# Performance work log

Hardware: AMD Instinct MI355X
Metric: run time of the kernel (lower is better)

The kernel has to match this reference:

```python
import itertools
import jax, jax.numpy as jnp
import numpy as np


def setup_inputs() -> dict:
    key = jax.random.key(0)
    k1, k2 = jax.random.split(key)
    # vol: [B, D, H, W, C]; flow: [B, D, H, W, 3] (dense displacement field, 'ij' indexing)
    vol = jax.random.normal(k1, (2, 160, 192, 160, 2), dtype=jnp.float32)
    flow = jax.random.normal(k2, (2, 160, 192, 160, 3), dtype=jnp.float32)
    return {"vol": vol, "flow": flow}


def _warp_single(vol, flow):
    """Trilinear warp of one volume. vol: [D,H,W,C], flow: [D,H,W,3]."""
    D, H, W, C = vol.shape
    nb_dims = 3
    # identity grid ('ij' indexing) + displacement -> sample locations
    gd, gh, gw = jnp.meshgrid(jnp.arange(D), jnp.arange(H), jnp.arange(W), indexing="ij")
    mesh = jnp.stack([gd, gh, gw], axis=-1).astype(flow.dtype)  # [D,H,W,3]
    loc = mesh + flow                                            # [D,H,W,3]

    max_loc = jnp.array([D - 1, H - 1, W - 1], dtype=loc.dtype)  # per-dim clamp
    loc0 = jnp.clip(jnp.floor(loc), 0.0, max_loc)                # lower corner (clipped)
    loc1 = jnp.clip(loc0 + 1.0, 0.0, max_loc)                    # upper corner (clipped)

    # linear weights: corner bit 0 -> (loc1 - loc), corner bit 1 -> 1 - (loc1 - loc)
    d1 = loc1 - loc   # weight when picking lower corner
    d0 = 1.0 - d1     # weight when picking upper corner

    i0 = loc0.astype(jnp.int32)  # [D,H,W,3]
    i1 = loc1.astype(jnp.int32)
    strides = (H * W, W, 1)
    vol_flat = vol.reshape(-1, C)  # [D*H*W, C]

    out = jnp.zeros((D, H, W, C), dtype=vol.dtype)
    for corner in itertools.product([0, 1], repeat=nb_dims):
        idx = 0
        wt = 1.0
        for d in range(nb_dims):
            ii = (i1 if corner[d] else i0)[..., d]
            idx = idx + ii * strides[d]
            wt = wt * (d0 if corner[d] else d1)[..., d]
        out = out + wt[..., None] * vol_flat[idx]  # gather [D,H,W,C]
    return out


def reference(vol, flow):
    # batch map over [B, ...] volumes, matching SpatialTransformer.call with a dense flow
    return jax.vmap(_warp_single)(vol, flow)
```

## Files before the change

kernel.cpp:

```cpp
#include <hip/hip_runtime.h>


constexpr int Bb = 2, Dd = 160, Hh = 192, Ww = 160;
constexpr int HW  = Hh * Ww;
constexpr int VOX = Dd * HW;

constexpr int TD = 8,  TH = 16, TW = 16;
constexpr int RD = TD + 8;
constexpr int RH = TH + 8;
constexpr int RW = TW + 8;
constexpr int RWP = 24;
constexpr int QROW = RW / 2;
constexpr int NQ = RD * RH * QROW;
constexpr int ND = Dd / TD, NH = Hh / TH, NW = Ww / TW;
constexpr int NBLK = Bb * ND * NH * NW;
constexpr int BLOCK = 1024;
constexpr size_t LDS_BYTES = (size_t)NQ * 16;

__device__ __forceinline__ void sample_global(const float2* __restrict__ v2,
                                              int d, int h, int w,
                                              float fx, float fy, float fz,
                                              float& oxv, float& oyv)
{
    const float mx = (float)(Dd - 1), my = (float)(Hh - 1), mz = (float)(Ww - 1);
    const float lxf = (float)d + fx;
    const float lyf = (float)h + fy;
    const float lzf = (float)w + fz;

    const float l0x = fminf(fmaxf(floorf(lxf), 0.0f), mx);
    const float l0y = fminf(fmaxf(floorf(lyf), 0.0f), my);
    const float l0z = fminf(fmaxf(floorf(lzf), 0.0f), mz);
    const float l1x = fminf(l0x + 1.0f, mx);
    const float l1y = fminf(l0y + 1.0f, my);
    const float l1z = fminf(l0z + 1.0f, mz);

    const float d1x = l1x - lxf, d0x = 1.0f - d1x;
    const float d1y = l1y - lyf, d0y = 1.0f - d1y;
    const float d1z = l1z - lzf, d0z = 1.0f - d1z;

    const int i0x = (int)l0x, i1x = (int)l1x;
    const int i0y = (int)l0y, i1y = (int)l1y;
    const int i0z = (int)l0z, i1z = (int)l1z;

    const int rx0 = i0x * HW, rx1 = i1x * HW;
    const int ry0 = i0y * Ww, ry1 = i1y * Ww;
    const float2 c000 = v2[rx0 + ry0 + i0z], c001 = v2[rx0 + ry0 + i1z];
    const float2 c010 = v2[rx0 + ry1 + i0z], c011 = v2[rx0 + ry1 + i1z];
    const float2 c100 = v2[rx1 + ry0 + i0z], c101 = v2[rx1 + ry0 + i1z];
    const float2 c110 = v2[rx1 + ry1 + i0z], c111 = v2[rx1 + ry1 + i1z];

    const float w000 = d1x * d1y * d1z, w001 = d1x * d1y * d0z;
    const float w010 = d1x * d0y * d1z, w011 = d1x * d0y * d0z;
    const float w100 = d0x * d1y * d1z, w101 = d0x * d1y * d0z;
    const float w110 = d0x * d0y * d1z, w111 = d0x * d0y * d0z;

    oxv = w000 * c000.x;
    oyv = w000 * c000.y;
    oxv = fmaf(w001, c001.x, oxv);  oyv = fmaf(w001, c001.y, oyv);
    oxv = fmaf(w010, c010.x, oxv);  oyv = fmaf(w010, c010.y, oyv);
    oxv = fmaf(w011, c011.x, oxv);  oyv = fmaf(w011, c011.y, oyv);
    oxv = fmaf(w100, c100.x, oxv);  oyv = fmaf(w100, c100.y, oyv);
    oxv = fmaf(w101, c101.x, oxv);  oyv = fmaf(w101, c101.y, oyv);
    oxv = fmaf(w110, c110.x, oxv);  oyv = fmaf(w110, c110.y, oyv);
    oxv = fmaf(w111, c111.x, oxv);  oyv = fmaf(w111, c111.y, oyv);
}

__global__ __launch_bounds__(BLOCK, 8)
void SpatialTransformer_44418551776013_kernel(const float* __restrict__ vol,
                                              const float* __restrict__ flow,
                                              float* __restrict__ out)
{
    extern __shared__ float2 sv[];
    const int tid = threadIdx.x;

    constexpr int CPX = NBLK / 8;
    int bid = (int)(blockIdx.x % 8) * CPX + (int)(blockIdx.x / 8);

    const int bw = bid % NW;  bid /= NW;
    const int bh = bid % NH;  bid /= NH;
    const int bd = bid % ND;
    const int b  = bid / ND;
    const int d0 = bd * TD, h0 = bh * TH, w0 = bw * TW;

    const int ox = max(0, d0 - 4), oy = max(0, h0 - 4), oz = max(0, w0 - 4);
    const int ex = min(Dd - 1, d0 + TD + 3) - ox + 1;
    const int ey = min(Hh - 1, h0 + TH + 3) - oy + 1;
    const int ez = min(Ww - 1, w0 + TW + 3) - oz + 1;
    const int qz = ez >> 1;

    const int tw2 = tid & 7;
    const int th  = (tid >> 3) & 15;
    const int td  = tid >> 7;
    const int h = h0 + th;
    const int w = w0 + 2 * tw2;
    const int d = d0 + td;
    const int gidx = ((b * Dd + d) * Hh + h) * Ww + w;

    const float4 fA = *reinterpret_cast<const float4*>(flow + (size_t)gidx * 3);
    const float2 fB = *reinterpret_cast<const float2*>(flow + (size_t)gidx * 3 + 4);

    const float2* __restrict__ v2 =
        reinterpret_cast<const float2*>(vol) + (size_t)b * VOX;

    if ((ex == RD) & (ey == RH) & (ez == RW)) {
        #pragma unroll 1
        for (int k = 0; k < 5; ++k) {
            const int i = tid + k * BLOCK;
            if (i < NQ) {
                const int lq = i % QROW;
                const int t  = i / QROW;
                const int ly = t % RH;
                const int lx = t / RH;
                const float2* src =
                    v2 + ((size_t)(ox + lx) * HW + (oy + ly) * Ww + oz + 2 * lq);
                __builtin_amdgcn_global_load_lds(
                    (const __attribute__((address_space(1))) void*)src,
                    (__attribute__((address_space(3))) void*)(sv + (size_t)2 * i),
                    16, 0, 0);
            }
        }
    } else {
        #pragma unroll 1
        for (int k = 0; k < 5; ++k) {
            const int i = tid + k * BLOCK;
            if (i < NQ) {
                int lq = i % QROW;
                const int t  = i / QROW;
                int ly = t % RH;
                int lx = t / RH;
                lx = min(lx, ex - 1);  ly = min(ly, ey - 1);  lq = min(lq, qz - 1);
                const float2* src =
                    v2 + ((size_t)(ox + lx) * HW + (oy + ly) * Ww + oz + 2 * lq);
                __builtin_amdgcn_global_load_lds(
                    (const __attribute__((address_space(1))) void*)src,
                    (__attribute__((address_space(3))) void*)(sv + (size_t)2 * i),
                    16, 0, 0);
            }
        }
    }
    __syncthreads();

    auto sample_lds = [&](int dd, int ww, float fx, float fy, float fz,
                          float& oxv, float& oyv, bool& ok) {
        const float mn3 = fminf(fminf(fx, fy), fz);
        const float mx3 = fmaxf(fmaxf(fx, fy), fz);
        ok = (mn3 >= -4.0f) & (mx3 < 4.0f);

        const float lxf = (float)dd + fx;
        const float lyf = (float)h  + fy;
        const float lzf = (float)ww + fz;

        const int i0x = min(max(__float2int_rd(lxf), 0), Dd - 1);
        const int i0y = min(max(__float2int_rd(lyf), 0), Hh - 1);
        const int i0z = min(max(__float2int_rd(lzf), 0), Ww - 1);
        const int i1x = min(i0x + 1, Dd - 1);
        const int i1y = min(i0y + 1, Hh - 1);
        const int i1z = min(i0z + 1, Ww - 1);

        const float d1x = (float)i1x - lxf, d0x = 1.0f - d1x;
        const float d1y = (float)i1y - lyf, d0y = 1.0f - d1y;
        const float d1z = (float)i1z - lzf, d0z = 1.0f - d1z;

        const int a0x = i0x - ox, a1x = i1x - ox;
        const int a0y = i0y - oy, a1y = i1y - oy;
        const int a0z = i0z - oz, a1z = i1z - oz;

        const int r00 = (a0x * RH + a0y) * RWP;
        const int r01 = (a0x * RH + a1y) * RWP;
        const int r10 = (a1x * RH + a0y) * RWP;
        const int r11 = (a1x * RH + a1y) * RWP;
        const float2 c000 = sv[r00 + a0z], c001 = sv[r00 + a1z];
        const float2 c010 = sv[r01 + a0z], c011 = sv[r01 + a1z];
        const float2 c100 = sv[r10 + a0z], c101 = sv[r10 + a1z];
        const float2 c110 = sv[r11 + a0z], c111 = sv[r11 + a1z];

        const float xy00 = d1x * d1y, xy01 = d1x * d0y;
        const float xy10 = d0x * d1y, xy11 = d0x * d0y;
        const float w000 = xy00 * d1z, w001 = xy00 * d0z;
        const float w010 = xy01 * d1z, w011 = xy01 * d0z;
        const float w100 = xy10 * d1z, w101 = xy10 * d0z;
        const float w110 = xy11 * d1z, w111 = xy11 * d0z;

        oxv = w000 * c000.x;
        oyv = w000 * c000.y;
        oxv = fmaf(w001, c001.x, oxv);  oyv = fmaf(w001, c001.y, oyv);
        oxv = fmaf(w010, c010.x, oxv);  oyv = fmaf(w010, c010.y, oyv);
        oxv = fmaf(w011, c011.x, oxv);  oyv = fmaf(w011, c011.y, oyv);
        oxv = fmaf(w100, c100.x, oxv);  oyv = fmaf(w100, c100.y, oyv);
        oxv = fmaf(w101, c101.x, oxv);  oyv = fmaf(w101, c101.y, oyv);
        oxv = fmaf(w110, c110.x, oxv);  oyv = fmaf(w110, c110.y, oyv);
        oxv = fmaf(w111, c111.x, oxv);  oyv = fmaf(w111, c111.y, oyv);
    };

    float o1x, o1y, o2x, o2y;
    bool ok1, ok2;
    sample_lds(d, w,     fA.x, fA.y, fA.z, o1x, o1y, ok1);
    sample_lds(d, w + 1, fA.w, fB.x, fB.y, o2x, o2y, ok2);

    if (!__all(ok1 && ok2)) {
        if (!ok1) sample_global(v2, d, h, w,     fA.x, fA.y, fA.z, o1x, o1y);
        if (!ok2) sample_global(v2, d, h, w + 1, fA.w, fB.x, fB.y, o2x, o2y);
    }

    *reinterpret_cast<float4*>(reinterpret_cast<float2*>(out) + gidx) =
        make_float4(o1x, o1y, o2x, o2y);
}

extern "C" void kernel_launch(void* const* d_in, const int* in_sizes, int n_in,
                              void* d_out, int out_size, void* d_ws, size_t ws_size,
                              hipStream_t stream)
{
    const float* vol  = (const float*)d_in[0];
    const float* flow = (const float*)d_in[1];
    float* out = (float*)d_out;

    SpatialTransformer_44418551776013_kernel<<<NBLK, BLOCK, LDS_BYTES, stream>>>(vol, flow, out);
}
```

Measured before the change: 65.27 us.

## Convert to persistent kernel with double-buffered LDS tile staging

Replaces the one-tile-per-block launch with a persistent grid of 256 blocks, each walking a contiguous range of about 18–19 tiles. While the current tile is sampled, the next tile's volume halo is prefetched asynchronously into a second LDS buffer with global_load_lds, along with its flow values. Hand-placed s_waitcnt plus barriers order the two buffers. The goal is to hide the staging load latency behind interpolation work. In exchange, LDS per block doubles to about 147KB, allowing only one 16-wave block per CU. The kernel also drops the old interleaved block-to-XCD mapping.

```diff
diff --git a/kernel.cpp b/kernel.cpp
--- a/kernel.cpp
+++ b/kernel.cpp
@@ -12,47 +12,124 @@
 constexpr int RWP = 24;
 constexpr int QROW = RW / 2;
 constexpr int NQ = RD * RH * QROW;
+constexpr int BUF2 = NQ * 2;
 constexpr int ND = Dd / TD, NH = Hh / TH, NW = Ww / TW;
-constexpr int NBLK = Bb * ND * NH * NW;
+constexpr int NTILE = Bb * ND * NH * NW;
 constexpr int BLOCK = 1024;
-constexpr size_t LDS_BYTES = (size_t)NQ * 16;
-
-__device__ __forceinline__ void sample_global(const float2* __restrict__ v2,
-                                              int d, int h, int w,
-                                              float fx, float fy, float fz,
-                                              float& oxv, float& oyv)
-{
-    const float mx = (float)(Dd - 1), my = (float)(Hh - 1), mz = (float)(Ww - 1);
-    const float lxf = (float)d + fx;
-    const float lyf = (float)h + fy;
-    const float lzf = (float)w + fz;
-
-    const float l0x = fminf(fmaxf(floorf(lxf), 0.0f), mx);
-    const float l0y = fminf(fmaxf(floorf(lyf), 0.0f), my);
-    const float l0z = fminf(fmaxf(floorf(lzf), 0.0f), mz);
-    const float l1x = fminf(l0x + 1.0f, mx);
-    const float l1y = fminf(l0y + 1.0f, my);
-    const float l1z = fminf(l0z + 1.0f, mz);
-
-    const float d1x = l1x - lxf, d0x = 1.0f - d1x;
-    const float d1y = l1y - lyf, d0y = 1.0f - d1y;
-    const float d1z = l1z - lzf, d0z = 1.0f - d1z;
-
-    const int i0x = (int)l0x, i1x = (int)l1x;
-    const int i0y = (int)l0y, i1y = (int)l1y;
-    const int i0z = (int)l0z, i1z = (int)l1z;
-
-    const int rx0 = i0x * HW, rx1 = i1x * HW;
-    const int ry0 = i0y * Ww, ry1 = i1y * Ww;
-    const float2 c000 = v2[rx0 + ry0 + i0z], c001 = v2[rx0 + ry0 + i1z];
-    const float2 c010 = v2[rx0 + ry1 + i0z], c011 = v2[rx0 + ry1 + i1z];
-    const float2 c100 = v2[rx1 + ry0 + i0z], c101 = v2[rx1 + ry0 + i1z];
-    const float2 c110 = v2[rx1 + ry1 + i0z], c111 = v2[rx1 + ry1 + i1z];
-
-    const float w000 = d1x * d1y * d1z, w001 = d1x * d1y * d0z;
-    const float w010 = d1x * d0y * d1z, w011 = d1x * d0y * d0z;
-    const float w100 = d0x * d1y * d1z, w101 = d0x * d1y * d0z;
-    const float w110 = d0x * d0y * d1z, w111 = d0x * d0y * d0z;
+constexpr int GRID  = 256;
+constexpr size_t LDS_BYTES = (size_t)BUF2 * 2 * sizeof(float2);
+
+struct Ctx {
+    int ox, oy, oz, ex, ey, ez, qz;
+    int d, h, w, gidx;
+    const float2* v2b;
+};
+
+__device__ __forceinline__ Ctx decode(int t, int tw2, int th, int td,
+                                      const float2* __restrict__ v2base)
+{
+    Ctx c;
+    const int bw = t % NW;  int r = t / NW;
+    const int bh = r % NH;  r /= NH;
+    const int bd = r % ND;  const int b = r / ND;
+    const int d0 = bd * TD, h0 = bh * TH, w0 = bw * TW;
+    c.ox = max(0, d0 - 4);  c.oy = max(0, h0 - 4);  c.oz = max(0, w0 - 4);
+    c.ex = min(Dd - 1, d0 + TD + 3) - c.ox + 1;
+    c.ey = min(Hh - 1, h0 + TH + 3) - c.oy + 1;
+    c.ez = min(Ww - 1, w0 + TW + 3) - c.oz + 1;
+    c.qz = c.ez >> 1;
+    c.d = d0 + td;  c.h = h0 + th;  c.w = w0 + 2 * tw2;
+    c.gidx = ((b * Dd + c.d) * Hh + c.h) * Ww + c.w;
+    c.v2b = v2base + (size_t)b * VOX;
+    return c;
+}
+
+__device__ __forceinline__ void stage(const Ctx& c, float2* __restrict__ dst,
+                                      int tid)
+{
+    if ((c.ex == RD) & (c.ey == RH) & (c.ez == RW)) {
+        #pragma unroll 1
+        for (int k = 0; k < 5; ++k) {
+            const int i = tid + k * BLOCK;
+            if (i < NQ) {
+                const int lq = i % QROW;
+                const int t  = i / QROW;
+                const int ly = t % RH;
+                const int lx = t / RH;
+                const float2* src = c.v2b +
+                    ((size_t)(c.ox + lx) * HW + (c.oy + ly) * Ww + c.oz + 2 * lq);
+                __builtin_amdgcn_global_load_lds(
+                    (const __attribute__((address_space(1))) void*)src,
+                    (__attribute__((address_space(3))) void*)(dst + (size_t)2 * i),
+                    16, 0, 0);
+            }
+        }
+    } else {
+        #pragma unroll 1
+        for (int k = 0; k < 5; ++k) {
+            const int i = tid + k * BLOCK;
+            if (i < NQ) {
+                int lq = i % QROW;
+                const int t  = i / QROW;
+                int ly = t % RH;
+                int lx = t / RH;
+                lx = min(lx, c.ex - 1);  ly = min(ly, c.ey - 1);
+                lq = min(lq, c.qz - 1);
+                const float2* src = c.v2b +
+                    ((size_t)(c.ox + lx) * HW + (c.oy + ly) * Ww + c.oz + 2 * lq);
+                __builtin_amdgcn_global_load_lds(
+                    (const __attribute__((address_space(1))) void*)src,
+                    (__attribute__((address_space(3))) void*)(dst + (size_t)2 * i),
+                    16, 0, 0);
+            }
+        }
+    }
+}
+
+__device__ __forceinline__ void sample_lds_f(const float2* __restrict__ buf,
+                                             int ox, int oy, int oz,
+                                             int dd, int hh, int ww,
+                                             float fx, float fy, float fz,
+                                             float& oxv, float& oyv, bool& ok)
+{
+    const float mn3 = fminf(fminf(fx, fy), fz);
+    const float mx3 = fmaxf(fmaxf(fx, fy), fz);
+    ok = (mn3 >= -4.0f) & (mx3 < 4.0f);
+
+    const float lxf = (float)dd + fx;
+    const float lyf = (float)hh + fy;
+    const float lzf = (float)ww + fz;
+
+    const int i0x = min(max(__float2int_rd(lxf), 0), Dd - 1);
+    const int i0y = min(max(__float2int_rd(lyf), 0), Hh - 1);
+    const int i0z = min(max(__float2int_rd(lzf), 0), Ww - 1);
+    const int i1x = min(i0x + 1, Dd - 1);
+    const int i1y = min(i0y + 1, Hh - 1);
+    const int i1z = min(i0z + 1, Ww - 1);
+
+    const float d1x = (float)i1x - lxf, d0x = 1.0f - d1x;
+    const float d1y = (float)i1y - lyf, d0y = 1.0f - d1y;
+    const float d1z = (float)i1z - lzf, d0z = 1.0f - d1z;
+
+    const int a0x = i0x - ox, a1x = i1x - ox;
+    const int a0y = i0y - oy, a1y = i1y - oy;
+    const int a0z = i0z - oz, a1z = i1z - oz;
+
+    const int r00 = (a0x * RH + a0y) * RWP;
+    const int r01 = (a0x * RH + a1y) * RWP;
+    const int r10 = (a1x * RH + a0y) * RWP;
+    const int r11 = (a1x * RH + a1y) * RWP;
+    const float2 c000 = buf[r00 + a0z], c001 = buf[r00 + a1z];
+    const float2 c010 = buf[r01 + a0z], c011 = buf[r01 + a1z];
+    const float2 c100 = buf[r10 + a0z], c101 = buf[r10 + a1z];
+    const float2 c110 = buf[r11 + a0z], c111 = buf[r11 + a1z];
+
+    const float xy00 = d1x * d1y, xy01 = d1x * d0y;
+    const float xy10 = d0x * d1y, xy11 = d0x * d0y;
+    const float w000 = xy00 * d1z, w001 = xy00 * d0z;
+    const float w010 = xy01 * d1z, w011 = xy01 * d0z;
+    const float w100 = xy10 * d1z, w101 = xy10 * d0z;
+    const float w110 = xy11 * d1z, w111 = xy11 * d0z;
 
     oxv = w000 * c000.x;
     oyv = w000 * c000.y;
@@ -65,145 +142,115 @@
     oxv = fmaf(w111, c111.x, oxv);  oyv = fmaf(w111, c111.y, oyv);
 }
 
-__global__ __launch_bounds__(BLOCK, 8)
+__device__ __forceinline__ void sample_global(const float2* __restrict__ v2,
+                                              int d, int h, int w,
+                                              float fx, float fy, float fz,
+                                              float& oxv, float& oyv)
+{
+    const float mx = (float)(Dd - 1), my = (float)(Hh - 1), mz = (float)(Ww - 1);
+    const float lxf = (float)d + fx;
+    const float lyf = (float)h + fy;
+    const float lzf = (float)w + fz;
+
+    const float l0x = fminf(fmaxf(floorf(lxf), 0.0f), mx);
+    const float l0y = fminf(fmaxf(floorf(lyf), 0.0f), my);
+    const float l0z = fminf(fmaxf(floorf(lzf), 0.0f), mz);
+    const float l1x = fminf(l0x + 1.0f, mx);
+    const float l1y = fminf(l0y + 1.0f, my);
+    const float l1z = fminf(l0z + 1.0f, mz);
+
+    const float d1x = l1x - lxf, d0x = 1.0f - d1x;
+    const float d1y = l1y - lyf, d0y = 1.0f - d1y;
+    const float d1z = l1z - lzf, d0z = 1.0f - d1z;
+
+    const int i0x = (int)l0x, i1x = (int)l1x;
+    const int i0y = (int)l0y, i1y = (int)l1y;
+    const int i0z = (int)l0z, i1z = (int)l1z;
+
+    const int rx0 = i0x * HW, rx1 = i1x * HW;
+    const int ry0 = i0y * Ww, ry1 = i1y * Ww;
+    const float2 c000 = v2[rx0 + ry0 + i0z], c001 = v2[rx0 + ry0 + i1z];
+    const float2 c010 = v2[rx0 + ry1 + i0z], c011 = v2[rx0 + ry1 + i1z];
+    const float2 c100 = v2[rx1 + ry0 + i0z], c101 = v2[rx1 + ry0 + i1z];
+    const float2 c110 = v2[rx1 + ry1 + i0z], c111 = v2[rx1 + ry1 + i1z];
+
+    const float w000 = d1x * d1y * d1z, w001 = d1x * d1y * d0z;
+    const float w010 = d1x * d0y * d1z, w011 = d1x * d0y * d0z;
+    const float w100 = d0x * d1y * d1z, w101 = d0x * d1y * d0z;
+    const float w110 = d0x * d0y * d1z, w111 = d0x * d0y * d0z;
+
+    oxv = w000 * c000.x;
+    oyv = w000 * c000.y;
+    oxv = fmaf(w001, c001.x, oxv);  oyv = fmaf(w001, c001.y, oyv);
+    oxv = fmaf(w010, c010.x, oxv);  oyv = fmaf(w010, c010.y, oyv);
+    oxv = fmaf(w011, c011.x, oxv);  oyv = fmaf(w011, c011.y, oyv);
+    oxv = fmaf(w100, c100.x, oxv);  oyv = fmaf(w100, c100.y, oyv);
+    oxv = fmaf(w101, c101.x, oxv);  oyv = fmaf(w101, c101.y, oyv);
+    oxv = fmaf(w110, c110.x, oxv);  oyv = fmaf(w110, c110.y, oyv);
+    oxv = fmaf(w111, c111.x, oxv);  oyv = fmaf(w111, c111.y, oyv);
+}
+
+__global__ __launch_bounds__(BLOCK, 4)
 void SpatialTransformer_44418551776013_kernel(const float* __restrict__ vol,
                                               const float* __restrict__ flow,
                                               float* __restrict__ out)
 {
     extern __shared__ float2 sv[];
     const int tid = threadIdx.x;
-
-    constexpr int CPX = NBLK / 8;
-    int bid = (int)(blockIdx.x % 8) * CPX + (int)(blockIdx.x / 8);
-
-    const int bw = bid % NW;  bid /= NW;
-    const int bh = bid % NH;  bid /= NH;
-    const int bd = bid % ND;
-    const int b  = bid / ND;
-    const int d0 = bd * TD, h0 = bh * TH, w0 = bw * TW;
-
-    const int ox = max(0, d0 - 4), oy = max(0, h0 - 4), oz = max(0, w0 - 4);
-    const int ex = min(Dd - 1, d0 + TD + 3) - ox + 1;
-    const int ey = min(Hh - 1, h0 + TH + 3) - oy + 1;
-    const int ez = min(Ww - 1, w0 + TW + 3) - oz + 1;
-    const int qz = ez >> 1;
-
     const int tw2 = tid & 7;
     const int th  = (tid >> 3) & 15;
     const int td  = tid >> 7;
-    const int h = h0 + th;
-    const int w = w0 + 2 * tw2;
-    const int d = d0 + td;
-    const int gidx = ((b * Dd + d) * Hh + h) * Ww + w;
-
-    const float4 fA = *reinterpret_cast<const float4*>(flow + (size_t)gidx * 3);
-    const float2 fB = *reinterpret_cast<const float2*>(flow + (size_t)gidx * 3 + 4);
-
-    const float2* __restrict__ v2 =
-        reinterpret_cast<const float2*>(vol) + (size_t)b * VOX;
-
-    if ((ex == RD) & (ey == RH) & (ez == RW)) {
-        #pragma unroll 1
-        for (int k = 0; k < 5; ++k) {
-            const int i = tid + k * BLOCK;
-            if (i < NQ) {
-                const int lq = i % QROW;
-                const int t  = i / QROW;
-                const int ly = t % RH;
-                const int lx = t / RH;
-                const float2* src =
-                    v2 + ((size_t)(ox + lx) * HW + (oy + ly) * Ww + oz + 2 * lq);
-                __builtin_amdgcn_global_load_lds(
-                    (const __attribute__((address_space(1))) void*)src,
-                    (__attribute__((address_space(3))) void*)(sv + (size_t)2 * i),
-                    16, 0, 0);
-            }
-        }
-    } else {
-        #pragma unroll 1
-        for (int k = 0; k < 5; ++k) {
-            const int i = tid + k * BLOCK;
-            if (i < NQ) {
-                int lq = i % QROW;
-                const int t  = i / QROW;
-                int ly = t % RH;
-                int lx = t / RH;
-                lx = min(lx, ex - 1);  ly = min(ly, ey - 1);  lq = min(lq, qz - 1);
-                const float2* src =
-                    v2 + ((size_t)(ox + lx) * HW + (oy + ly) * Ww + oz + 2 * lq);
-                __builtin_amdgcn_global_load_lds(
-                    (const __attribute__((address_space(1))) void*)src,
-                    (__attribute__((address_space(3))) void*)(sv + (size_t)2 * i),
-                    16, 0, 0);
-            }
-        }
+
+    const float2* __restrict__ v2base = reinterpret_cast<const float2*>(vol);
+
+    const int bi    = blockIdx.x;
+    const int tbase = bi * 18 + min(bi, 192);
+    const int tcnt  = 18 + (bi < 192 ? 1 : 0);
+
+    Ctx ccur = decode(tbase, tw2, th, td, v2base);
+    float4 fAc = *reinterpret_cast<const float4*>(flow + (size_t)ccur.gidx * 3);
+    float2 fBc = *reinterpret_cast<const float2*>(flow + (size_t)ccur.gidx * 3 + 4);
+    stage(ccur, sv, tid);
+
+    Ctx ctxn = ccur;
+    float4 fAn = fAc;  float2 fBn = fBc;
+
+    #pragma unroll 1
+    for (int k = 0; k < tcnt; ++k) {
+        if (k == 0) { asm volatile("s_waitcnt vmcnt(0)" ::: "memory"); }
+        else        { asm volatile("s_waitcnt vmcnt(1)" ::: "memory"); }
+        __builtin_amdgcn_sched_barrier(0);
+        __builtin_amdgcn_s_barrier();
+        asm volatile("" ::: "memory");
+        __builtin_amdgcn_sched_barrier(0);
+
+        if (k + 1 < tcnt) {
+            ctxn = decode(tbase + k + 1, tw2, th, td, v2base);
+            fAn = *reinterpret_cast<const float4*>(flow + (size_t)ctxn.gidx * 3);
+            fBn = *reinterpret_cast<const float2*>(flow + (size_t)ctxn.gidx * 3 + 4);
+            stage(ctxn, sv + (size_t)((k + 1) & 1) * BUF2, tid);
+        }
+
+        const float2* __restrict__ buf = sv + (size_t)(k & 1) * BUF2;
+        float o1x, o1y, o2x, o2y;
+        bool ok1, ok2;
+        sample_lds_f(buf, ccur.ox, ccur.oy, ccur.oz, ccur.d, ccur.h, ccur.w,
+                     fAc.x, fAc.y, fAc.z, o1x, o1y, ok1);
+        sample_lds_f(buf, ccur.ox, ccur.oy, ccur.oz, ccur.d, ccur.h, ccur.w + 1,
+                     fAc.w, fBc.x, fBc.y, o2x, o2y, ok2);
+
+        if (!__all(ok1 && ok2)) {
+            if (!ok1) sample_global(ccur.v2b, ccur.d, ccur.h, ccur.w,
+                                    fAc.x, fAc.y, fAc.z, o1x, o1y);
+            if (!ok2) sample_global(ccur.v2b, ccur.d, ccur.h, ccur.w + 1,
+                                    fAc.w, fBc.x, fBc.y, o2x, o2y);
+        }
+
+        *reinterpret_cast<float4*>(reinterpret_cast<float2*>(out) + ccur.gidx) =
+            make_float4(o1x, o1y, o2x, o2y);
+
+        ccur = ctxn;  fAc = fAn;  fBc = fBn;
     }
-    __syncthreads();
-
-    auto sample_lds = [&](int dd, int ww, float fx, float fy, float fz,
-                          float& oxv, float& oyv, bool& ok) {
-        const float mn3 = fminf(fminf(fx, fy), fz);
-        const float mx3 = fmaxf(fmaxf(fx, fy), fz);
-        ok = (mn3 >= -4.0f) & (mx3 < 4.0f);
-
-        const float lxf = (float)dd + fx;
-        const float lyf = (float)h  + fy;
-        const float lzf = (float)ww + fz;
-
-        const int i0x = min(max(__float2int_rd(lxf), 0), Dd - 1);
-        const int i0y = min(max(__float2int_rd(lyf), 0), Hh - 1);
-        const int i0z = min(max(__float2int_rd(lzf), 0), Ww - 1);
-        const int i1x = min(i0x + 1, Dd - 1);
-        const int i1y = min(i0y + 1, Hh - 1);
-        const int i1z = min(i0z + 1, Ww - 1);
-
-        const float d1x = (float)i1x - lxf, d0x = 1.0f - d1x;
-        const float d1y = (float)i1y - lyf, d0y = 1.0f - d1y;
-        const float d1z = (float)i1z - lzf, d0z = 1.0f - d1z;
-
-        const int a0x = i0x - ox, a1x = i1x - ox;
-        const int a0y = i0y - oy, a1y = i1y - oy;
-        const int a0z = i0z - oz, a1z = i1z - oz;
-
-        const int r00 = (a0x * RH + a0y) * RWP;
-        const int r01 = (a0x * RH + a1y) * RWP;
-        const int r10 = (a1x * RH + a0y) * RWP;
-        const int r11 = (a1x * RH + a1y) * RWP;
-        const float2 c000 = sv[r00 + a0z], c001 = sv[r00 + a1z];
-        const float2 c010 = sv[r01 + a0z], c011 = sv[r01 + a1z];
-        const float2 c100 = sv[r10 + a0z], c101 = sv[r10 + a1z];
-        const float2 c110 = sv[r11 + a0z], c111 = sv[r11 + a1z];
-
-        const float xy00 = d1x * d1y, xy01 = d1x * d0y;
-        const float xy10 = d0x * d1y, xy11 = d0x * d0y;
-        const float w000 = xy00 * d1z, w001 = xy00 * d0z;
-        const float w010 = xy01 * d1z, w011 = xy01 * d0z;
-        const float w100 = xy10 * d1z, w101 = xy10 * d0z;
-        const float w110 = xy11 * d1z, w111 = xy11 * d0z;
-
-        oxv = w000 * c000.x;
-        oyv = w000 * c000.y;
-        oxv = fmaf(w001, c001.x, oxv);  oyv = fmaf(w001, c001.y, oyv);
-        oxv = fmaf(w010, c010.x, oxv);  oyv = fmaf(w010, c010.y, oyv);
-        oxv = fmaf(w011, c011.x, oxv);  oyv = fmaf(w011, c011.y, oyv);
-        oxv = fmaf(w100, c100.x, oxv);  oyv = fmaf(w100, c100.y, oyv);
-        oxv = fmaf(w101, c101.x, oxv);  oyv = fmaf(w101, c101.y, oyv);
-        oxv = fmaf(w110, c110.x, oxv);  oyv = fmaf(w110, c110.y, oyv);
-        oxv = fmaf(w111, c111.x, oxv);  oyv = fmaf(w111, c111.y, oyv);
-    };
-
-    float o1x, o1y, o2x, o2y;
-    bool ok1, ok2;
-    sample_lds(d, w,     fA.x, fA.y, fA.z, o1x, o1y, ok1);
-    sample_lds(d, w + 1, fA.w, fB.x, fB.y, o2x, o2y, ok2);
-
-    if (!__all(ok1 && ok2)) {
-        if (!ok1) sample_global(v2, d, h, w,     fA.x, fA.y, fA.z, o1x, o1y);
-        if (!ok2) sample_global(v2, d, h, w + 1, fA.w, fB.x, fB.y, o2x, o2y);
-    }
-
-    *reinterpret_cast<float4*>(reinterpret_cast<float2*>(out) + gidx) =
-        make_float4(o1x, o1y, o2x, o2y);
 }
 
 extern "C" void kernel_launch(void* const* d_in, const int* in_sizes, int n_in,
@@ -214,5 +261,5 @@
     const float* flow = (const float*)d_in[1];
     float* out = (float*)d_out;
 
-    SpatialTransformer_44418551776013_kernel<<<NBLK, BLOCK, LDS_BYTES, stream>>>(vol, flow, out);
-}
+    SpatialTransformer_44418551776013_kernel<<<GRID, BLOCK, LDS_BYTES, stream>>>(vol, flow, out);
+}
```

Measured after the change: 119.5 us. +83.1%, slower.
